# Kernel tuning notes

Measured on AMD Instinct MI355X. Metric: run time of the kernel, lower is better.

## Reference

```python
import jax, jax.numpy as jnp
import numpy as np

B, N, E = 32, 128, 16384
D, H, O, A = 72, 72, 72, 4   # n_input, n_hidden, n_output, n_node_attr
C_WEIGHT = 1.0
EPS = 1e-5  # BatchNorm1d default eps


def setup_inputs() -> dict:
    key = jax.random.key(0)
    ks = jax.random.split(key, 16)
    rn = lambda k, shp, s=0.05: jax.random.normal(k, shp, jnp.float32) * s
    return {
        "h": jax.random.normal(ks[0], (B, N, D), jnp.float32),
        "x": jax.random.normal(ks[1], (B, N, 4), jnp.float32),
        "edgei": jax.random.randint(ks[2], (B, E), 0, N),
        "edgej": jax.random.randint(ks[3], (B, E), 0, N),
        "node_attr": jax.random.normal(ks[4], (B, N, A), jnp.float32),
        # phi_e: Linear(2D+2 -> H, no bias), BN, ReLU, Linear(H->H), ReLU
        "We1": rn(ks[5], (2 * D + 2, H)),
        "g1": jnp.ones((H,), jnp.float32), "b1": jnp.zeros((H,), jnp.float32),
        "We2": rn(ks[6], (H, H)), "be2": jnp.zeros((H,), jnp.float32),
        # phi_m: Linear(H->1), Sigmoid
        "Wm": rn(ks[7], (H, 1)), "bm": jnp.zeros((1,), jnp.float32),
        # phi_x: Linear(H->H), ReLU, Linear(H->1, no bias, tiny init)
        "Wx1": rn(ks[8], (H, H)), "bx1": jnp.zeros((H,), jnp.float32),
        "Wx2": rn(ks[9], (H, 1), 0.001),
        # phi_h: Linear(H+D+A -> H), BN, ReLU, Linear(H->O)
        "Wh1": rn(ks[10], (H + D + A, H)), "bh1": jnp.zeros((H,), jnp.float32),
        "gh": jnp.ones((H,), jnp.float32), "bh": jnp.zeros((H,), jnp.float32),
        "Wh2": rn(ks[11], (H, O)), "bh2": jnp.zeros((O,), jnp.float32),
    }


def _psi(p):
    return jnp.sign(p) * jnp.log1p(jnp.abs(p))


def _normsq4(p):  # Minkowski norm: p0^2 - p1^2 - p2^2 - p3^2
    psq = p * p
    return 2.0 * psq[..., 0] - psq.sum(axis=-1)


def _dotsq4(p, q):  # Minkowski inner product
    pq = p * q
    return 2.0 * pq[..., 0] - pq.sum(axis=-1)


def _batchnorm(z, g, b):  # training-mode BatchNorm1d over flattened batch dim
    mu = z.mean(axis=0)
    var = z.var(axis=0)
    return (z - mu) * jax.lax.rsqrt(var + EPS) * g + b


_seg_sum = jax.vmap(lambda d, s: jax.ops.segment_sum(d, s, num_segments=N))


def reference(h, x, edgei, edgej, node_attr,
              We1, g1, b1, We2, be2, Wm, bm,
              Wx1, bx1, Wx2, Wh1, bh1, gh, bh, Wh2, bh2):
    # gather edge endpoint features (equiv. to torch.gather along dim 1)
    xi = jnp.take_along_axis(x, edgei[:, :, None], axis=1)    # [B,E,4]
    xj = jnp.take_along_axis(x, edgej[:, :, None], axis=1)
    hi = jnp.take_along_axis(h, edgei[:, :, None], axis=1)    # [B,E,D]
    hj = jnp.take_along_axis(h, edgej[:, :, None], axis=1)
    x_diff = xi - xj
    norms = _psi(_normsq4(x_diff))[..., None]                 # [B,E,1]
    dots = _psi(_dotsq4(xi, xj))[..., None]                   # [B,E,1]

    # m_model: phi_e then sigmoid gate phi_m
    feat = jnp.concatenate([hi, hj, norms, dots], axis=-1)    # [B,E,2D+2]
    z = feat.reshape(-1, 2 * D + 2) @ We1
    z = jax.nn.relu(_batchnorm(z, g1, b1))
    z = jax.nn.relu(z @ We2 + be2)
    m = z.reshape(B, E, H)
    m = m * jax.nn.sigmoid(m @ Wm + bm)                       # gated messages

    # x_model: equivariant coordinate update (segment mean over edges)
    gate = jax.nn.relu(m @ Wx1 + bx1) @ Wx2                   # [B,E,1]
    trans = jnp.clip(x_diff * gate, -100.0, 100.0)
    agg = _seg_sum(trans, edgei)                              # [B,N,4]
    cnt = _seg_sum(jnp.ones_like(trans), edgei)
    x_out = x + (agg / jnp.maximum(cnt, 1.0)) * C_WEIGHT

    # h_model: segment sum of messages, node MLP, residual
    magg = _seg_sum(m, edgei)                                 # [B,N,H]
    hin = jnp.concatenate([h, magg, node_attr], axis=-1).reshape(-1, H + D + A)
    z2 = hin @ Wh1 + bh1
    z2 = jax.nn.relu(_batchnorm(z2, gh, bh))
    z2 = z2 @ Wh2 + bh2
    h_out = h + z2.reshape(B, N, O)

    return (h_out, x_out, m)
```

## Files before the change

kernel.cpp:

```cpp
#include <hip/hip_runtime.h>

#define BB 32
#define NN 128
#define EE 16384
#define ROWS_E (BB*EE)
#define ROWS_N (BB*NN)
#define EPS_BN 1e-5f

#define XOUT_OFF (ROWS_N*72)
#define M_OFF    (XOUT_OFF + ROWS_N*4)

#define ST1_OFF 0
#define ST2_OFF 512
#define AGG_OFF 1024
#define CNT_OFF (AGG_OFF + ROWS_N*4)
#define MAGG_OFF (CNT_OFF + ROWS_N)
#define Z2_OFF (MAGG_OFF + ROWS_N*72)
#define ZERO_FLOATS Z2_OFF
#define WB_OFF (Z2_OFF + ROWS_N*72)

#define WE1T_OFF 0
#define WE2T_OFF 13440
#define WX1T_OFF 21760
#define WH1T_OFF 30080
#define WH2T_OFF 43520
#define WB_TOTAL 51840

#define SS 168

typedef __attribute__((ext_vector_type(8))) short short8;
typedef __attribute__((ext_vector_type(4))) float f32x4;

__device__ __forceinline__ float psi_f(float p) {
    return copysignf(log1pf(fabsf(p)), p);
}
__device__ __forceinline__ unsigned short f2bf(float f) {
    union { float f; unsigned u; } v; v.f = f;
    unsigned r = v.u + 0x7fffu + ((v.u >> 16) & 1u);
    return (unsigned short)(r >> 16);
}
__device__ __forceinline__ unsigned pk(float a, float b) {
    return (unsigned)f2bf(a) | ((unsigned)f2bf(b) << 16);
}

__global__ void k_prep(const float* __restrict__ We1, const float* __restrict__ We2,
                       const float* __restrict__ Wx1, const float* __restrict__ Wh1,
                       const float* __restrict__ Wh2, unsigned short* __restrict__ wb)
{
    int idx = blockIdx.x * 256 + threadIdx.x;
    if (idx >= WB_TOTAL) return;
    const float* src; int off, n, k, K;
    if (idx < WE2T_OFF)      { off = idx;            n = off/168; k = off%168; src = We1; K = 146; }
    else if (idx < WH1T_OFF && idx >= WX1T_OFF) { off = idx - WX1T_OFF; n = off/104; k = off%104; src = Wx1; K = 72; }
    else if (idx < WX1T_OFF) { off = idx - WE2T_OFF; n = off/104; k = off%104; src = We2; K = 72; }
    else if (idx < WH2T_OFF) { off = idx - WH1T_OFF; n = off/168; k = off%168; src = Wh1; K = 148; }
    else                     { off = idx - WH2T_OFF; n = off/104; k = off%104; src = Wh2; K = 72; }
    float v = (n < 72 && k < K) ? src[k * 72 + n] : 0.f;
    wb[idx] = f2bf(v);
}

__device__ __forceinline__ void stage_feat(
    unsigned short* At, const float* __restrict__ h, const float* __restrict__ x,
    const int* __restrict__ ei, const int* __restrict__ ej, int tid, int blk)
{
    int rl = tid >> 1, half = tid & 1;
    int row = blk * 128 + rl;
    int b = row >> 14;
    int i = ei[row], j = ej[row];
    int node = half ? j : i;
    const float4* hp = (const float4*)(h + (size_t)(b * 128 + node) * 72);
    uint2* arow = (uint2*)(&At[rl * SS + half * 72]);
    #pragma unroll
    for (int q = 0; q < 18; q++) {
        float4 v = hp[q];
        arow[q] = make_uint2(pk(v.x, v.y), pk(v.z, v.w));
    }
    if (half == 0) {
        float4 xi = *(const float4*)(x + (size_t)(b * 128 + i) * 4);
        float4 xj = *(const float4*)(x + (size_t)(b * 128 + j) * 4);
        float d0 = xi.x - xj.x, d1 = xi.y - xj.y, d2 = xi.z - xj.z, d3 = xi.w - xj.w;
        float nrm = d0*d0 - d1*d1 - d2*d2 - d3*d3;
        float dot = xi.x*xj.x - xi.y*xj.y - xi.z*xj.z - xi.w*xj.w;
        *(unsigned*)(&At[rl * SS + 144]) = pk(psi_f(nrm), psi_f(dot));
        unsigned* tp = (unsigned*)(&At[rl * SS + 146]);
        tp[0] = 0u; tp[1] = 0u; tp[2] = 0u;
    } else {
        unsigned* tp = (unsigned*)(&At[rl * SS + 152]);
        tp[0] = 0u; tp[1] = 0u; tp[2] = 0u; tp[3] = 0u;
    }
}

__global__ __launch_bounds__(256, 3) void k_edge_stats(
    const float* __restrict__ h, const float* __restrict__ x,
    const int* __restrict__ ei, const int* __restrict__ ej,
    const unsigned short* __restrict__ We1t, float* __restrict__ st)
{
    __shared__ unsigned short At[128 * SS];
    int tid = threadIdx.x;
    stage_feat(At, h, x, ei, ej, tid, blockIdx.x);

    int wv = tid >> 6, lane = tid & 63, c = lane & 15, quad = lane >> 4;
    f32x4 acc[2][5] = {};
    for (int kc = 0; kc < 5; kc++) {
        int k0 = kc * 32 + quad * 8;
        short8 a0 = *(const short8*)(&At[(wv * 32 + c) * SS + k0]);
        short8 a1 = *(const short8*)(&At[(wv * 32 + 16 + c) * SS + k0]);
        #pragma unroll
        for (int ct = 0; ct < 5; ct++) {
            short8 bf = *(const short8*)(&We1t[(ct * 16 + c) * 168 + k0]);
            acc[0][ct] = __builtin_amdgcn_mfma_f32_16x16x32_bf16(a0, bf, acc[0][ct], 0, 0, 0);
            acc[1][ct] = __builtin_amdgcn_mfma_f32_16x16x32_bf16(a1, bf, acc[1][ct], 0, 0, 0);
        }
    }
    float* sredw = (float*)(&At[wv * 32 * SS]);
    #pragma unroll
    for (int ct = 0; ct < 5; ct++) {
        int col = ct * 16 + c;
        float s = 0.f, q = 0.f;
        #pragma unroll
        for (int rt = 0; rt < 2; rt++)
            #pragma unroll
            for (int r = 0; r < 4; r++) {
                float v = acc[rt][ct][r];
                s += v; q += v * v;
            }
        s += __shfl_xor(s, 16); s += __shfl_xor(s, 32);
        q += __shfl_xor(q, 16); q += __shfl_xor(q, 32);
        if (lane < 16 && col < 72) { sredw[col] = s; sredw[72 + col] = q; }
    }
    __syncthreads();
    if (tid < 144) {
        const float* a = (const float*)At;
        atomicAdd(&st[tid], a[tid] + a[2688 + tid] + a[5376 + tid] + a[8064 + tid]);
    }
}

__global__ void k_finalize(float* __restrict__ st, float inv_rows)
{
    int c = threadIdx.x;
    if (c < 72) {
        float mean = st[c] * inv_rows;
        float var  = st[72 + c] * inv_rows - mean * mean;
        st[144 + c] = mean;
        st[216 + c] = rsqrtf(var + EPS_BN);
    }
}

__global__ __launch_bounds__(256, 3) void k_edge_fused(
    const float* __restrict__ h, const float* __restrict__ x,
    const int* __restrict__ ei, const int* __restrict__ ej,
    const float* __restrict__ st1, const float* __restrict__ g1, const float* __restrict__ b1,
    const float* __restrict__ be2, const float* __restrict__ Wm, const float* __restrict__ bm,
    const float* __restrict__ bx1, const float* __restrict__ Wx2,
    const unsigned short* __restrict__ We1t, const unsigned short* __restrict__ We2t,
    const unsigned short* __restrict__ Wx1t,
    float* __restrict__ m, float* __restrict__ agg, float* __restrict__ cnt,
    float* __restrict__ magg)
{
    __shared__ unsigned short At[128 * SS];
    int tid = threadIdx.x;
    stage_feat(At, h, x, ei, ej, tid, blockIdx.x);

    int wv = tid >> 6, lane = tid & 63, c = lane & 15, quad = lane >> 4;
    f32x4 acc1[2][5] = {};
    for (int kc = 0; kc < 5; kc++) {
        int k0 = kc * 32 + quad * 8;
        short8 a0 = *(const short8*)(&At[(wv * 32 + c) * SS + k0]);
        short8 a1 = *(const short8*)(&At[(wv * 32 + 16 + c) * SS + k0]);
        #pragma unroll
        for (int ct = 0; ct < 5; ct++) {
            short8 bf = *(const short8*)(&We1t[(ct * 16 + c) * 168 + k0]);
            acc1[0][ct] = __builtin_amdgcn_mfma_f32_16x16x32_bf16(a0, bf, acc1[0][ct], 0, 0, 0);
            acc1[1][ct] = __builtin_amdgcn_mfma_f32_16x16x32_bf16(a1, bf, acc1[1][ct], 0, 0, 0);
        }
    }
    const float* mean = st1 + 144;
    const float* inv  = st1 + 216;
    #pragma unroll
    for (int ct = 0; ct < 5; ct++) {
        int col = ct * 16 + c;
        float mu = 0.f, iv = 0.f, ga = 0.f, be = 0.f;
        if (col < 72) { mu = mean[col]; iv = inv[col]; ga = g1[col]; be = b1[col]; }
        #pragma unroll
        for (int rt = 0; rt < 2; rt++)
            #pragma unroll
            for (int r = 0; r < 4; r++) {
                float a = (col < 72) ? fmaxf((acc1[rt][ct][r] - mu) * iv * ga + be, 0.f) : 0.f;
                int lrow = wv * 32 + rt * 16 + quad * 4 + r;
                At[lrow * SS + col] = f2bf(a);
            }
    }
    {
        int r_ = lane >> 1, h_ = lane & 1;
        uint* zp = (uint*)&At[(wv * 32 + r_) * SS + 80 + h_ * 8];
        zp[0] = 0u; zp[1] = 0u; zp[2] = 0u; zp[3] = 0u;
    }
    f32x4 acc2[2][5] = {};
    for (int kc = 0; kc < 3; kc++) {
        int k0 = kc * 32 + quad * 8;
        short8 a0 = *(const short8*)(&At[(wv * 32 + c) * SS + k0]);
        short8 a1 = *(const short8*)(&At[(wv * 32 + 16 + c) * SS + k0]);
        #pragma unroll
        for (int ct = 0; ct < 5; ct++) {
            short8 bf = *(const short8*)(&We2t[(ct * 16 + c) * 104 + k0]);
            acc2[0][ct] = __builtin_amdgcn_mfma_f32_16x16x32_bf16(a0, bf, acc2[0][ct], 0, 0, 0);
            acc2[1][ct] = __builtin_amdgcn_mfma_f32_16x16x32_bf16(a1, bf, acc2[1][ct], 0, 0, 0);
        }
    }
    float part[2][4] = {};
    float bm0 = bm[0];
    #pragma unroll
    for (int ct = 0; ct < 5; ct++) {
        int col = ct * 16 + c;
        float bias = (col < 72) ? be2[col] : 0.f;
        float wm   = (col < 72) ? Wm[col]  : 0.f;
        #pragma unroll
        for (int rt = 0; rt < 2; rt++)
            #pragma unroll
            for (int r = 0; r < 4; r++) {
                float t = fmaxf(acc2[rt][ct][r] + bias, 0.f);
                acc2[rt][ct][r] = t;
                part[rt][r] += t * wm;
            }
    }
    float sg[2][4];
    #pragma unroll
    for (int rt = 0; rt < 2; rt++)
        #pragma unroll
        for (int r = 0; r < 4; r++) {
            float s = part[rt][r];
            s += __shfl_xor(s, 1); s += __shfl_xor(s, 2);
            s += __shfl_xor(s, 4); s += __shfl_xor(s, 8);
            sg[rt][r] = 1.f / (1.f + expf(-(s + bm0)));
        }
    size_t rbase = (size_t)blockIdx.x * 128 + wv * 32 + quad * 4;
    int bb = blockIdx.x >> 7;
    int nd[2][4];
    #pragma unroll
    for (int rt = 0; rt < 2; rt++)
        #pragma unroll
        for (int r = 0; r < 4; r++)
            nd[rt][r] = ei[rbase + rt * 16 + r];
    #pragma unroll
    for (int rt = 0; rt < 2; rt++)
        #pragma unroll
        for (int ct = 0; ct < 5; ct++) {
            int col = ct * 16 + c;
            #pragma unroll
            for (int r = 0; r < 4; r++) {
                float mv = acc2[rt][ct][r] * sg[rt][r];
                int lrow = wv * 32 + rt * 16 + quad * 4 + r;
                At[lrow * SS + col] = f2bf(mv);
                if (col < 72) {
                    m[(rbase + rt * 16 + r) * 72 + col] = mv;
                    atomicAdd(&magg[(size_t)(bb * 128 + nd[rt][r]) * 72 + col], mv);
                }
            }
        }
    f32x4 acc3[2][5] = {};
    for (int kc = 0; kc < 3; kc++) {
        int k0 = kc * 32 + quad * 8;
        short8 a0 = *(const short8*)(&At[(wv * 32 + c) * SS + k0]);
        short8 a1 = *(const short8*)(&At[(wv * 32 + 16 + c) * SS + k0]);
        #pragma unroll
        for (int ct = 0; ct < 5; ct++) {
            short8 bf = *(const short8*)(&Wx1t[(ct * 16 + c) * 104 + k0]);
            acc3[0][ct] = __builtin_amdgcn_mfma_f32_16x16x32_bf16(a0, bf, acc3[0][ct], 0, 0, 0);
            acc3[1][ct] = __builtin_amdgcn_mfma_f32_16x16x32_bf16(a1, bf, acc3[1][ct], 0, 0, 0);
        }
    }
    float part3[2][4] = {};
    #pragma unroll
    for (int ct = 0; ct < 5; ct++) {
        int col = ct * 16 + c;
        float bias = (col < 72) ? bx1[col] : 0.f;
        float wx   = (col < 72) ? Wx2[col] : 0.f;
        #pragma unroll
        for (int rt = 0; rt < 2; rt++)
            #pragma unroll
            for (int r = 0; r < 4; r++)
                part3[rt][r] += fmaxf(acc3[rt][ct][r] + bias, 0.f) * wx;
    }
    float* gp = (float*)&At[(wv * 32) * SS + 96];
    #pragma unroll
    for (int rt = 0; rt < 2; rt++)
        #pragma unroll
        for (int r = 0; r < 4; r++) {
            float s = part3[rt][r];
            s += __shfl_xor(s, 1); s += __shfl_xor(s, 2);
            s += __shfl_xor(s, 4); s += __shfl_xor(s, 8);
            if (c == 0) gp[rt * 16 + quad * 4 + r] = s;
        }
    __syncthreads();
    if (tid < 128) {
        size_t erow = (size_t)blockIdx.x * 128 + tid;
        int b = (int)(erow >> 14);
        int i2 = ei[erow], j2 = ej[erow];
        float g2 = *((float*)&At[((tid >> 5) * 32) * SS + 96] + (tid & 31));
        float4 xi = *(const float4*)(x + (size_t)(b * 128 + i2) * 4);
        float4 xj = *(const float4*)(x + (size_t)(b * 128 + j2) * 4);
        float t0 = fminf(fmaxf((xi.x - xj.x) * g2, -100.f), 100.f);
        float t1 = fminf(fmaxf((xi.y - xj.y) * g2, -100.f), 100.f);
        float t2 = fminf(fmaxf((xi.z - xj.z) * g2, -100.f), 100.f);
        float t3 = fminf(fmaxf((xi.w - xj.w) * g2, -100.f), 100.f);
        float* ap = agg + (size_t)(b * 128 + i2) * 4;
        atomicAdd(ap + 0, t0); atomicAdd(ap + 1, t1);
        atomicAdd(ap + 2, t2); atomicAdd(ap + 3, t3);
        atomicAdd(cnt + (size_t)(b * 128 + i2), 1.f);
    }
}

__global__ __launch_bounds__(256) void k_node_gemm1(
    const float* __restrict__ h, const float* __restrict__ node_attr,
    const float* __restrict__ magg, const unsigned short* __restrict__ Wh1t,
    const float* __restrict__ bh1, float* __restrict__ z2, float* __restrict__ st)
{
    __shared__ unsigned short At[128 * 168];
    __shared__ unsigned short Wt[80 * 168];
    __shared__ float sred[4][144];
    int tid = threadIdx.x;
    {
        const uint4* s = (const uint4*)Wh1t; uint4* d = (uint4*)Wt;
        for (int q = tid; q < 1680; q += 256) d[q] = s[q];
    }
    int rl = tid >> 1, half = tid & 1;
    size_t row = (size_t)blockIdx.x * 128 + rl;
    const float4* sp = (const float4*)((half ? magg : h) + row * 72);
    uint2* arow = (uint2*)(&At[rl * 168 + half * 72]);
    #pragma unroll
    for (int q = 0; q < 18; q++) {
        float4 v = sp[q];
        arow[q] = make_uint2(pk(v.x, v.y), pk(v.z, v.w));
    }
    if (half) {
        float4 na = *(const float4*)(node_attr + row * 4);
        *(unsigned*)(&At[rl * 168 + 144]) = pk(na.x, na.y);
        *(unsigned*)(&At[rl * 168 + 146]) = pk(na.z, na.w);
        unsigned* tailp = (unsigned*)(&At[rl * 168 + 148]);
        #pragma unroll
        for (int q = 0; q < 10; q++) tailp[q] = 0u;
    }
    __syncthreads();

    int wv = tid >> 6, lane = tid & 63, c = lane & 15, quad = lane >> 4;
    f32x4 acc[2][5] = {};
    for (int kc = 0; kc < 5; kc++) {
        int k0 = kc * 32 + quad * 8;
        short8 a0 = *(const short8*)(&At[(wv * 32 + c) * 168 + k0]);
        short8 a1 = *(const short8*)(&At[(wv * 32 + 16 + c) * 168 + k0]);
        #pragma unroll
        for (int ct = 0; ct < 5; ct++) {
            short8 bf = *(const short8*)(&Wt[(ct * 16 + c) * 168 + k0]);
            acc[0][ct] = __builtin_amdgcn_mfma_f32_16x16x32_bf16(a0, bf, acc[0][ct], 0, 0, 0);
            acc[1][ct] = __builtin_amdgcn_mfma_f32_16x16x32_bf16(a1, bf, acc[1][ct], 0, 0, 0);
        }
    }
    size_t rbase = (size_t)blockIdx.x * 128 + wv * 32 + quad * 4;
    #pragma unroll
    for (int ct = 0; ct < 5; ct++) {
        int col = ct * 16 + c;
        float bias = (col < 72) ? bh1[col] : 0.f;
        float s = 0.f, q = 0.f;
        #pragma unroll
        for (int rt = 0; rt < 2; rt++) {
            float* op = z2 + (rbase + rt * 16) * 72 + col;
            #pragma unroll
            for (int r = 0; r < 4; r++) {
                float v = acc[rt][ct][r] + bias;
                if (col < 72) op[(size_t)r * 72] = v;
                s += v; q += v * v;
            }
        }
        s += __shfl_xor(s, 16); s += __shfl_xor(s, 32);
        q += __shfl_xor(q, 16); q += __shfl_xor(q, 32);
        if (lane < 16 && col < 72) { sred[wv][col] = s; sred[wv][72 + col] = q; }
    }
    __syncthreads();
    if (tid < 144)
        atomicAdd(&st[tid], sred[0][tid] + sred[1][tid] + sred[2][tid] + sred[3][tid]);
}

__global__ __launch_bounds__(256) void k_node_final(
    const float* __restrict__ h, const float* __restrict__ x,
    const float* __restrict__ z2, const float* __restrict__ st2,
    const float* __restrict__ gh, const float* __restrict__ bh,
    const unsigned short* __restrict__ Wh2t, const float* __restrict__ bh2,
    const float* __restrict__ agg, const float* __restrict__ cnt,
    float* __restrict__ hout, float* __restrict__ xout)
{
    __shared__ unsigned short Zt[128 * 104];
    __shared__ unsigned short Wt[80 * 104];
    int tid = threadIdx.x;
    {
        const uint4* s = (const uint4*)Wh2t; uint4* d = (uint4*)Wt;
        for (int q = tid; q < 1040; q += 256) d[q] = s[q];
    }
    int rl = tid >> 1, half = tid & 1;
    size_t row = (size_t)blockIdx.x * 128 + rl;
    const float* mean = st2 + 144;
    const float* inv  = st2 + 216;
    const float4* zp = (const float4*)(z2 + row * 72) + half * 9;
    uint2* arow = (uint2*)(&Zt[rl * 104 + half * 36]);
    #pragma unroll
    for (int q = 0; q < 9; q++) {
        int k = half * 36 + q * 4;
        float4 v = zp[q];
        float a0 = fmaxf((v.x - mean[k  ]) * inv[k  ] * gh[k  ] + bh[k  ], 0.f);
        float a1 = fmaxf((v.y - mean[k+1]) * inv[k+1] * gh[k+1] + bh[k+1], 0.f);
        float a2 = fmaxf((v.z - mean[k+2]) * inv[k+2] * gh[k+2] + bh[k+2], 0.f);
        float a3 = fmaxf((v.w - mean[k+3]) * inv[k+3] * gh[k+3] + bh[k+3], 0.f);
        arow[q] = make_uint2(pk(a0, a1), pk(a2, a3));
    }
    uint2* prow = (uint2*)(&Zt[rl * 104]);
    #pragma unroll
    for (int q = 0; q < 4; q++) prow[18 + half * 4 + q] = make_uint2(0u, 0u);
    __syncthreads();

    int wv = tid >> 6, lane = tid & 63, c = lane & 15, quad = lane >> 4;
    f32x4 acc[2][5] = {};
    for (int kc = 0; kc < 3; kc++) {
        int k0 = kc * 32 + quad * 8;
        short8 a0 = *(const short8*)(&Zt[(wv * 32 + c) * 104 + k0]);
        short8 a1 = *(const short8*)(&Zt[(wv * 32 + 16 + c) * 104 + k0]);
        #pragma unroll
        for (int ct = 0; ct < 5; ct++) {
            short8 bf = *(const short8*)(&Wt[(ct * 16 + c) * 104 + k0]);
            acc[0][ct] = __builtin_amdgcn_mfma_f32_16x16x32_bf16(a0, bf, acc[0][ct], 0, 0, 0);
            acc[1][ct] = __builtin_amdgcn_mfma_f32_16x16x32_bf16(a1, bf, acc[1][ct], 0, 0, 0);
        }
    }
    size_t rbase = (size_t)blockIdx.x * 128 + wv * 32 + quad * 4;
    #pragma unroll
    for (int rt = 0; rt < 2; rt++)
        #pragma unroll
        for (int ct = 0; ct < 5; ct++) {
            int col = ct * 16 + c;
            if (col < 72) {
                float bias = bh2[col];
                #pragma unroll
                for (int r = 0; r < 4; r++) {
                    size_t gr = (rbase + rt * 16 + r);
                    hout[gr * 72 + col] = h[gr * 72 + col] + acc[rt][ct][r] + bias;
                }
            }
        }
    if (tid < 128) {
        size_t nrow = (size_t)blockIdx.x * 128 + tid;
        float cn = fmaxf(cnt[nrow], 1.f);
        float4 ag = *(const float4*)(agg + nrow * 4);
        float4 xv = *(const float4*)(x + nrow * 4);
        ((float4*)xout)[nrow] = make_float4(xv.x + ag.x / cn, xv.y + ag.y / cn,
                                            xv.z + ag.z / cn, xv.w + ag.w / cn);
    }
}

extern "C" void kernel_launch(void* const* d_in, const int* in_sizes, int n_in,
                              void* d_out, int out_size, void* d_ws, size_t ws_size,
                              hipStream_t stream)
{
    const float* h   = (const float*)d_in[0];
    const float* x   = (const float*)d_in[1];
    const int*   ei  = (const int*)d_in[2];
    const int*   ej  = (const int*)d_in[3];
    const float* na  = (const float*)d_in[4];
    const float* We1 = (const float*)d_in[5];
    const float* g1  = (const float*)d_in[6];
    const float* b1  = (const float*)d_in[7];
    const float* We2 = (const float*)d_in[8];
    const float* be2 = (const float*)d_in[9];
    const float* Wm  = (const float*)d_in[10];
    const float* bm  = (const float*)d_in[11];
    const float* Wx1 = (const float*)d_in[12];
    const float* bx1 = (const float*)d_in[13];
    const float* Wx2 = (const float*)d_in[14];
    const float* Wh1 = (const float*)d_in[15];
    const float* bh1 = (const float*)d_in[16];
    const float* gh  = (const float*)d_in[17];
    const float* bhp = (const float*)d_in[18];
    const float* Wh2 = (const float*)d_in[19];
    const float* bh2 = (const float*)d_in[20];

    float* out  = (float*)d_out;
    float* hout = out;
    float* xout = out + XOUT_OFF;
    float* m    = out + M_OFF;
    float* ws   = (float*)d_ws;
    float* st1  = ws + ST1_OFF;
    float* st2  = ws + ST2_OFF;
    float* agg  = ws + AGG_OFF;
    float* cnt  = ws + CNT_OFF;
    float* magg = ws + MAGG_OFF;
    float* z2   = ws + Z2_OFF;
    unsigned short* wb = (unsigned short*)(ws + WB_OFF);

    hipMemsetAsync(d_ws, 0, (size_t)ZERO_FLOATS * sizeof(float), stream);
    k_prep<<<(WB_TOTAL + 255) / 256, 256, 0, stream>>>(We1, We2, Wx1, Wh1, Wh2, wb);
    k_edge_stats<<<ROWS_E / 128, 256, 0, stream>>>(h, x, ei, ej, wb + WE1T_OFF, st1);
    k_finalize<<<1, 128, 0, stream>>>(st1, 1.0f / (float)ROWS_E);
    k_edge_fused<<<ROWS_E / 128, 256, 0, stream>>>(h, x, ei, ej, st1, g1, b1, be2, Wm, bm,
                                                   bx1, Wx2, wb + WE1T_OFF, wb + WE2T_OFF,
                                                   wb + WX1T_OFF, m, agg, cnt, magg);
    k_node_gemm1<<<ROWS_N / 128, 256, 0, stream>>>(h, na, magg, wb + WH1T_OFF, bh1, z2, st2);
    k_finalize<<<1, 128, 0, stream>>>(st2, 1.0f / (float)ROWS_N);
    k_node_final<<<ROWS_N / 128, 256, 0, stream>>>(h, x, z2, st2, gh, bhp,
                                                   wb + WH2T_OFF, bh2, agg, cnt, hout, xout);
}
```

Measured before the change: 766.0 us.

## Move message segment-sum to separate LDS-privatized kernel and use hardware bf16 convert

Removes per-element global atomicAdd of gated messages into magg from the fused edge kernel. A new kernel re-reads m per batch chunk, accumulates into a shared-memory node table with LDS atomics, then flushes once per block with global atomics. This trades heavy global atomic contention for an extra read of the m tensor and another launch. The bf16 conversion helpers also switch to the packed hardware conversion instruction.

```diff
diff --git a/kernel.cpp b/kernel.cpp
--- a/kernel.cpp
+++ b/kernel.cpp
@@ -34,13 +34,15 @@
 __device__ __forceinline__ float psi_f(float p) {
     return copysignf(log1pf(fabsf(p)), p);
 }
+__device__ __forceinline__ unsigned pk(float a, float b) {
+    unsigned r;
+    asm("v_cvt_pk_bf16_f32 %0, %1, %2" : "=v"(r) : "v"(a), "v"(b));
+    return r;
+}
 __device__ __forceinline__ unsigned short f2bf(float f) {
-    union { float f; unsigned u; } v; v.f = f;
-    unsigned r = v.u + 0x7fffu + ((v.u >> 16) & 1u);
-    return (unsigned short)(r >> 16);
-}
-__device__ __forceinline__ unsigned pk(float a, float b) {
-    return (unsigned)f2bf(a) | ((unsigned)f2bf(b) << 16);
+    unsigned r;
+    asm("v_cvt_pk_bf16_f32 %0, %1, %1" : "=v"(r) : "v"(f));
+    return (unsigned short)r;
 }
 
 __global__ void k_prep(const float* __restrict__ We1, const float* __restrict__ We2,
@@ -154,8 +156,7 @@
     const float* __restrict__ bx1, const float* __restrict__ Wx2,
     const unsigned short* __restrict__ We1t, const unsigned short* __restrict__ We2t,
     const unsigned short* __restrict__ Wx1t,
-    float* __restrict__ m, float* __restrict__ agg, float* __restrict__ cnt,
-    float* __restrict__ magg)
+    float* __restrict__ m, float* __restrict__ agg, float* __restrict__ cnt)
 {
     __shared__ unsigned short At[128 * SS];
     int tid = threadIdx.x;
@@ -234,13 +235,6 @@
             sg[rt][r] = 1.f / (1.f + expf(-(s + bm0)));
         }
     size_t rbase = (size_t)blockIdx.x * 128 + wv * 32 + quad * 4;
-    int bb = blockIdx.x >> 7;
-    int nd[2][4];
-    #pragma unroll
-    for (int rt = 0; rt < 2; rt++)
-        #pragma unroll
-        for (int r = 0; r < 4; r++)
-            nd[rt][r] = ei[rbase + rt * 16 + r];
     #pragma unroll
     for (int rt = 0; rt < 2; rt++)
         #pragma unroll
@@ -251,10 +245,7 @@
                 float mv = acc2[rt][ct][r] * sg[rt][r];
                 int lrow = wv * 32 + rt * 16 + quad * 4 + r;
                 At[lrow * SS + col] = f2bf(mv);
-                if (col < 72) {
-                    m[(rbase + rt * 16 + r) * 72 + col] = mv;
-                    atomicAdd(&magg[(size_t)(bb * 128 + nd[rt][r]) * 72 + col], mv);
-                }
+                if (col < 72) m[(rbase + rt * 16 + r) * 72 + col] = mv;
             }
         }
     f32x4 acc3[2][5] = {};
@@ -308,6 +299,35 @@
         atomicAdd(ap + 2, t2); atomicAdd(ap + 3, t3);
         atomicAdd(cnt + (size_t)(b * 128 + i2), 1.f);
     }
+}
+
+__global__ __launch_bounds__(256, 4) void k_magg(
+    const float* __restrict__ m, const int* __restrict__ ei, float* __restrict__ magg)
+{
+    __shared__ float accum[128 * 72];
+    int tid = threadIdx.x;
+    for (int q = tid; q < 9216; q += 256) accum[q] = 0.f;
+    __syncthreads();
+    int b = blockIdx.x >> 5, chunk = blockIdx.x & 31;
+    int wv = tid >> 6, lane = tid & 63;
+    int ebase = b * 16384 + chunk * 512;
+    for (int e = wv; e < 512; e += 8) {
+        int e0 = ebase + e, e1 = ebase + e + 4;
+        int n0 = ei[e0], n1 = ei[e1];
+        const float* r0 = m + (size_t)e0 * 72;
+        const float* r1 = m + (size_t)e1 * 72;
+        float v0 = r0[lane];
+        float v1 = r1[lane];
+        float t0 = (lane < 8) ? r0[64 + lane] : 0.f;
+        float t1 = (lane < 8) ? r1[64 + lane] : 0.f;
+        atomicAdd(&accum[n0 * 72 + lane], v0);
+        if (lane < 8) atomicAdd(&accum[n0 * 72 + 64 + lane], t0);
+        atomicAdd(&accum[n1 * 72 + lane], v1);
+        if (lane < 8) atomicAdd(&accum[n1 * 72 + 64 + lane], t1);
+    }
+    __syncthreads();
+    float* mg = magg + (size_t)b * 9216;
+    for (int q = tid; q < 9216; q += 256) atomicAdd(&mg[q], accum[q]);
 }
 
 __global__ __launch_bounds__(256) void k_node_gemm1(
@@ -499,7 +519,8 @@
     k_finalize<<<1, 128, 0, stream>>>(st1, 1.0f / (float)ROWS_E);
     k_edge_fused<<<ROWS_E / 128, 256, 0, stream>>>(h, x, ei, ej, st1, g1, b1, be2, Wm, bm,
                                                    bx1, Wx2, wb + WE1T_OFF, wb + WE2T_OFF,
-                                                   wb + WX1T_OFF, m, agg, cnt, magg);
+                                                   wb + WX1T_OFF, m, agg, cnt);
+    k_magg<<<1024, 256, 0, stream>>>(m, ei, magg);
     k_node_gemm1<<<ROWS_N / 128, 256, 0, stream>>>(h, na, magg, wb + WH1T_OFF, bh1, z2, st2);
     k_finalize<<<1, 128, 0, stream>>>(st2, 1.0f / (float)ROWS_N);
     k_node_final<<<ROWS_N / 128, 256, 0, stream>>>(h, x, z2, st2, gh, bhp,
```

Measured after the change: 700.1 us. 8.6% less time.
